# Kernel optimization log

Hardware: AMD Instinct MI355X
Metric: run time of the kernel (lower is better)

## Reference

```python
import jax, jax.numpy as jnp
import numpy as np

EPS = 1e-4
HEADS = 16
DH = 64


def setup_inputs() -> dict:
    key = jax.random.key(0)
    ks = jax.random.split(key, 5)
    b, t, d = 2, 2048, 1024
    return {
        "X": jax.random.normal(ks[0], (b, t, d), dtype=jnp.float32),
        "W_in": jax.random.normal(ks[1], (HEADS * 4 * DH, d), dtype=jnp.float32) * (1.0 / np.sqrt(d)),
        "b_in": jax.random.normal(ks[2], (HEADS * 4 * DH,), dtype=jnp.float32) * 0.01,
        "W_out": jax.random.normal(ks[3], (d, HEADS * DH), dtype=jnp.float32) * (1.0 / np.sqrt(HEADS * DH)),
        "b_out": jax.random.normal(ks[4], (d,), dtype=jnp.float32) * 0.01,
    }


def reference(X, W_in, b_in, W_out, b_out):
    b, t, d = X.shape
    # project_in: [b,t,h*4*dh] -> [b,t,h,4*dh] -> [b,h,t,4*dh]
    P = jnp.einsum('btd,ed->bte', X, W_in) + b_in
    P = P.reshape(b, t, HEADS, 4 * DH).transpose(0, 2, 1, 3)
    Q, K, V, G = jnp.split(P, 4, axis=-1)  # each [b,h,t,dh]
    # Euclidean cdist: sqrt(||q||^2 + ||k||^2 - 2 q.k), clamped at 0
    q2 = jnp.sum(Q * Q, axis=-1)[..., :, None]   # [b,h,t,1]
    k2 = jnp.sum(K * K, axis=-1)[..., None, :]   # [b,h,1,t]
    qk = jnp.einsum('bhqd,bhkd->bhqk', Q, K)
    dist = jnp.sqrt(jnp.maximum(q2 + k2 - 2.0 * qk, 0.0))
    # Shepard weights: (eps + dist)^-2, normalized over keys
    W = (EPS + dist) ** (-2)
    W = W / (EPS + jnp.sum(W, axis=-1, keepdims=True))
    A = jnp.einsum('bhqk,bhkd->bhqd', W, V)
    # gate, merge heads: [b,h,t,dh] -> [b,t,h*dh]
    H = (G * A).transpose(0, 2, 1, 3).reshape(b, t, HEADS * DH)
    Y = jnp.einsum('bte,de->btd', H, W_out) + b_out
    return Y
```

## Files before the change

kernel.cpp:

```cpp
#include <hip/hip_runtime.h>
#include <math.h>

#define EPS 1e-4f


typedef __attribute__((ext_vector_type(8))) short bf16x8;
typedef __attribute__((ext_vector_type(8))) unsigned short u16x8;
typedef __attribute__((ext_vector_type(4))) float f32x4;

#define MFMA(a, b, c) __builtin_amdgcn_mfma_f32_16x16x32_bf16(a, b, c, 0, 0, 0)

__device__ __forceinline__ unsigned short f2b(float f) {
    unsigned int u = __float_as_uint(f);
    u += 0x7fffu + ((u >> 16) & 1u);
    return (unsigned short)(u >> 16);
}
__device__ __forceinline__ float b2f(unsigned short u) {
    return __uint_as_float(((unsigned int)u) << 16);
}
__device__ __forceinline__ unsigned int cvtpk(float a, float b) {
    unsigned int r;
    asm("v_cvt_pk_bf16_f32 %0, %1, %2" : "=v"(r) : "v"(a), "v"(b));
    return r;
}

typedef __attribute__((address_space(1))) const unsigned int as1_u32;
typedef __attribute__((address_space(3))) unsigned int as3_u32;
__device__ __forceinline__ void gl_lds16(const unsigned short* g, unsigned short* l) {
    __builtin_amdgcn_global_load_lds((as1_u32*)g, (as3_u32*)l, 16, 0, 0);
}

__global__ __launch_bounds__(256)
void sga_f2b(const float* __restrict__ src, unsigned short* __restrict__ dst, int n8) {
    int i = blockIdx.x * 256 + threadIdx.x;
    const int stride = gridDim.x * 256;
    for (; i < n8; i += stride) {
        const float4* s = (const float4*)src + i * 2;
        float4 a = s[0], b = s[1];
        uint4 o;
        o.x = (unsigned)f2b(a.x) | ((unsigned)f2b(a.y) << 16);
        o.y = (unsigned)f2b(a.z) | ((unsigned)f2b(a.w) << 16);
        o.z = (unsigned)f2b(b.x) | ((unsigned)f2b(b.y) << 16);
        o.w = (unsigned)f2b(b.z) | ((unsigned)f2b(b.w) << 16);
        *((uint4*)dst + i) = o;
    }
}

__global__ __launch_bounds__(256)
void sga_gemm1(const unsigned short* __restrict__ Xb, const unsigned short* __restrict__ Wb,
               const float* __restrict__ bin,
               unsigned short* __restrict__ Qb, unsigned short* __restrict__ Kb,
               unsigned short* __restrict__ Vt, unsigned short* __restrict__ Gb,
               float* __restrict__ q2s, float* __restrict__ k2s)
{
    __shared__ unsigned short As[128 * 64];
    __shared__ unsigned short Bs[128 * 64];
    const int tid = threadIdx.x;
    const int lane = tid & 63, w = tid >> 6;
    const int lr = lane & 15, lg = lane >> 4;
    const int wm = w & 1, wn = w >> 1;
    const int m0 = blockIdx.y * 128, n0 = blockIdx.x * 128;

    const int sr = tid >> 3, sc8 = tid & 7;
    const int gch = sc8 ^ (sr & 7);
    const unsigned short* aBase = Xb + (m0 + sr) * 1024 + gch * 8;
    const unsigned short* bBase = Wb + (n0 + sr) * 1024 + gch * 8;
    unsigned short* aDst = &As[w * 512];
    unsigned short* bDst = &Bs[w * 512];

    f32x4 acc[4][4] = {};

    for (int kt = 0; kt < 16; ++kt) {
        __syncthreads();
        #pragma unroll
        for (int c = 0; c < 4; ++c)
            gl_lds16(aBase + c * 32768 + kt * 64, aDst + c * 2048);
        #pragma unroll
        for (int c = 0; c < 4; ++c)
            gl_lds16(bBase + c * 32768 + kt * 64, bDst + c * 2048);
        __syncthreads();

        #pragma unroll
        for (int ks = 0; ks < 2; ++ks) {
            bf16x8 af[4], bfr[4];
            #pragma unroll
            for (int i = 0; i < 4; ++i) {
                const int row = wm * 64 + i * 16 + lr;
                af[i] = *(const bf16x8*)&As[row * 64 + (((ks * 4 + lg) ^ (row & 7)) * 8)];
            }
            #pragma unroll
            for (int i = 0; i < 4; ++i) {
                const int row = wn * 64 + i * 16 + lr;
                bfr[i] = *(const bf16x8*)&Bs[row * 64 + (((ks * 4 + lg) ^ (row & 7)) * 8)];
            }
            #pragma unroll
            for (int mi = 0; mi < 4; ++mi)
                #pragma unroll
                for (int ni = 0; ni < 4; ++ni)
                    acc[mi][ni] = MFMA(af[mi], bfr[ni], acc[mi][ni]);
        }
    }

    const int bb = m0 >> 11;
    const bool qkBlock = ((n0 & 128) == 0);
    #pragma unroll
    for (int mf = 0; mf < 4; ++mf) {
        const int tbase = m0 + wm * 64 + mf * 16 + lg * 4;
        const int tloc = tbase & 2047;
        float s2[4] = {0.f, 0.f, 0.f, 0.f};
        #pragma unroll
        for (int nf = 0; nf < 4; ++nf) {
            const int n = n0 + wn * 64 + nf * 16 + lr;
            const int h = n >> 8, cc = n & 255;
            const int part = cc >> 6, j = cc & 63;
            const int bh = bb * 16 + h;
            const float bz = bin[n];
            f32x4 v = acc[mf][nf];
            unsigned short e0 = f2b(v[0] + bz), e1 = f2b(v[1] + bz),
                           e2 = f2b(v[2] + bz), e3 = f2b(v[3] + bz);
            if (qkBlock) {
                float f0 = b2f(e0), f1 = b2f(e1), f2 = b2f(e2), f3 = b2f(e3);
                s2[0] += f0 * f0; s2[1] += f1 * f1;
                s2[2] += f2 * f2; s2[3] += f3 * f3;
            }
            if (part == 2) {
                ushort4 pk = make_ushort4(e0, e1, e2, e3);
                *(ushort4*)&Vt[(bh * 64 + j) * 2048 + tloc] = pk;
            } else {
                unsigned short* dst = (part == 0) ? Qb : ((part == 1) ? Kb : Gb);
                unsigned short vv[4] = {e0, e1, e2, e3};
                #pragma unroll
                for (int r = 0; r < 4; ++r)
                    dst[(bh * 2048 + tloc + r) * 64 + j] = vv[r];
            }
        }
        if (qkBlock) {
            const int bh = bb * 16 + (n0 >> 8);
            float* __restrict__ dstn = wn ? k2s : q2s;
            #pragma unroll
            for (int r = 0; r < 4; ++r) {
                float v = s2[r];
                v += __shfl_xor(v, 1, 64); v += __shfl_xor(v, 2, 64);
                v += __shfl_xor(v, 4, 64); v += __shfl_xor(v, 8, 64);
                if (lr == 0) dstn[bh * 2048 + ((tloc + r) & 2047)] = v;
            }
        }
    }
}

__global__ __launch_bounds__(256, 4)
void sga_attn(const unsigned short* __restrict__ Qb, const unsigned short* __restrict__ Kb,
              const unsigned short* __restrict__ Vt,
              const float* __restrict__ q2s, const float* __restrict__ k2s,
              unsigned short* __restrict__ Op0, unsigned short* __restrict__ Op1,
              unsigned short* __restrict__ Op2, unsigned short* __restrict__ Op3,
              float* __restrict__ Sw0, float* __restrict__ Sw1,
              float* __restrict__ Sw2, float* __restrict__ Sw3)
{
    __shared__ unsigned short Klds[4096];
    __shared__ unsigned short Vlds[4096];
    __shared__ unsigned short Wlds[4 * 2048];

    const int tid = threadIdx.x;
    const int lane = tid & 63, w = tid >> 6;
    const int lr = lane & 15, lg = lane >> 4;

    const int qt = blockIdx.x, bh = blockIdx.y, half = blockIdx.z;
    const int q0 = qt * 128 + w * 32;
    const int kbeg = half * 8, kend = kbeg + 8;

    unsigned short* wl = &Wlds[w * 2048];
    unsigned short* __restrict__ Op =
        (half & 2) ? ((half & 1) ? Op3 : Op2) : ((half & 1) ? Op1 : Op0);
    float* __restrict__ Sw =
        (half & 2) ? ((half & 1) ? Sw3 : Sw2) : ((half & 1) ? Sw1 : Sw0);

    const int sr8 = tid >> 3, sch = tid & 7;
    const int gch = sch ^ (sr8 & 7);
    const unsigned short* Kg = Kb + bh * 2048 * 64;
    const unsigned short* Vg = Vt + bh * 64 * 2048;
    unsigned short* kDst = &Klds[w * 512];
    unsigned short* vDst = &Vlds[w * 512];

    bf16x8 qf[2][2];
    #pragma unroll
    for (int g = 0; g < 2; ++g) {
        const unsigned short* qp = Qb + (bh * 2048 + q0 + g * 16 + lr) * 64 + lg * 8;
        qf[g][0] = *(const bf16x8*)qp;
        qf[g][1] = *(const bf16x8*)(qp + 32);
    }
    float q2v[2];
    q2v[0] = q2s[bh * 2048 + q0 + lr];
    q2v[1] = q2s[bh * 2048 + q0 + 16 + lr];

    f32x4 oacc[2][4] = {};
    float sumw[2] = {0.f, 0.f};

    for (int kt = kbeg; kt < kend; ++kt) {
        const int k0 = kt * 64;

        __syncthreads();
        #pragma unroll
        for (int c = 0; c < 2; ++c) {
            const int row = c * 32 + sr8;
            gl_lds16(Kg + (k0 + row) * 64 + gch * 8, kDst + c * 2048);
            gl_lds16(Vg + row * 2048 + k0 + gch * 8, vDst + c * 2048);
        }
        __syncthreads();

        f32x4 k2v[4];
        #pragma unroll
        for (int nf = 0; nf < 4; ++nf)
            k2v[nf] = *(const f32x4*)&k2s[bh * 2048 + k0 + nf * 16 + lg * 4];

        f32x4 sa[2][4] = {};
        __builtin_amdgcn_s_setprio(1);
        #pragma unroll
        for (int nf = 0; nf < 4; ++nf) {
            const int row = nf * 16 + lr;
            bf16x8 kf0 = *(const bf16x8*)&Klds[row * 64 + ((lg ^ (row & 7)) * 8)];
            bf16x8 kf1 = *(const bf16x8*)&Klds[row * 64 + (((4 + lg) ^ (row & 7)) * 8)];
            #pragma unroll
            for (int g = 0; g < 2; ++g) {
                sa[g][nf] = MFMA(kf0, qf[g][0], sa[g][nf]);
                sa[g][nf] = MFMA(kf1, qf[g][1], sa[g][nf]);
            }
        }
        __builtin_amdgcn_s_setprio(0);

        #pragma unroll
        for (int g = 0; g < 2; ++g) {
            const int row = g * 16 + lr;
            #pragma unroll
            for (int nf = 0; nf < 4; ++nf) {
                float wv[4];
                #pragma unroll
                for (int r = 0; r < 4; ++r) {
                    float d2 = fmaf(-2.0f, sa[g][nf][r], q2v[g] + k2v[nf][r]);
                    d2 = fmaxf(d2, 1e-8f);
                    wv[r] = __builtin_amdgcn_rcpf(d2);
                    sumw[g] += wv[r];
                }
                uint2 pk;
                pk.x = cvtpk(wv[0], wv[1]);
                pk.y = cvtpk(wv[2], wv[3]);
                const int c = 2 * nf + (lg >> 1);
                *(uint2*)&wl[row * 64 + ((c ^ (row & 7)) * 8) + (lg & 1) * 4] = pk;
            }
        }

        bf16x8 pa[2][2];
        #pragma unroll
        for (int g = 0; g < 2; ++g) {
            const int row = g * 16 + lr;
            pa[g][0] = *(const bf16x8*)&wl[row * 64 + ((lg ^ (row & 7)) * 8)];
            pa[g][1] = *(const bf16x8*)&wl[row * 64 + (((4 + lg) ^ (row & 7)) * 8)];
        }
        __builtin_amdgcn_s_setprio(1);
        #pragma unroll
        for (int vf = 0; vf < 4; ++vf) {
            const int row = vf * 16 + lr;
            bf16x8 v0 = *(const bf16x8*)&Vlds[row * 64 + ((lg ^ (row & 7)) * 8)];
            bf16x8 v1 = *(const bf16x8*)&Vlds[row * 64 + (((4 + lg) ^ (row & 7)) * 8)];
            #pragma unroll
            for (int g = 0; g < 2; ++g) {
                oacc[g][vf] = MFMA(pa[g][0], v0, oacc[g][vf]);
                oacc[g][vf] = MFMA(pa[g][1], v1, oacc[g][vf]);
            }
        }
        __builtin_amdgcn_s_setprio(0);
    }

    #pragma unroll
    for (int g = 0; g < 2; ++g) {
        sumw[g] += __shfl_xor(sumw[g], 16, 64);
        sumw[g] += __shfl_xor(sumw[g], 32, 64);
    }

    #pragma unroll
    for (int g = 0; g < 2; ++g) {
        #pragma unroll
        for (int vf = 0; vf < 4; ++vf) {
            #pragma unroll
            for (int r = 0; r < 4; ++r) {
                const int t = q0 + g * 16 + lg * 4 + r;
                const int dh = vf * 16 + lr;
                Op[(bh * 2048 + t) * 64 + dh] = f2b(oacc[g][vf][r]);
            }
        }
    }
    if (lg == 0) {
        Sw[bh * 2048 + q0 + lr]      = sumw[0];
        Sw[bh * 2048 + q0 + 16 + lr] = sumw[1];
    }
}

__global__ __launch_bounds__(256)
void sga_combine(const unsigned short* __restrict__ Op0, const unsigned short* __restrict__ Op1,
                 const unsigned short* __restrict__ Op2, const unsigned short* __restrict__ Op3,
                 const float* __restrict__ Sw0, const float* __restrict__ Sw1,
                 const float* __restrict__ Sw2, const float* __restrict__ Sw3,
                 const unsigned short* __restrict__ Gb, unsigned short* __restrict__ Hb)
{
    const int idx = blockIdx.x * 256 + threadIdx.x;
    const int t16 = idx >> 3;
    const int dq = (idx & 7) << 3;
    u16x8 a = *(const u16x8*)&Op0[t16 * 64 + dq];
    u16x8 b = *(const u16x8*)&Op1[t16 * 64 + dq];
    u16x8 c = *(const u16x8*)&Op2[t16 * 64 + dq];
    u16x8 d = *(const u16x8*)&Op3[t16 * 64 + dq];
    u16x8 g = *(const u16x8*)&Gb[t16 * 64 + dq];
    const float s = Sw0[t16] + Sw1[t16] + Sw2[t16] + Sw3[t16];
    const float inv = __builtin_amdgcn_rcpf(EPS + s);
    const int bh = t16 >> 11, tloc = t16 & 2047;
    const int bb = bh >> 4, h = bh & 15;
    u16x8 o;
    #pragma unroll
    for (int j = 0; j < 8; ++j)
        o[j] = f2b((b2f(a[j]) + b2f(b[j]) + b2f(c[j]) + b2f(d[j])) * inv * b2f(g[j]));
    *(u16x8*)&Hb[(bb * 2048 + tloc) * 1024 + h * 64 + dq] = o;
}

__global__ __launch_bounds__(256)
void sga_gemm2(const unsigned short* __restrict__ Hb, const unsigned short* __restrict__ Wb,
               const float* __restrict__ bout, float* __restrict__ Y)
{
    __shared__ unsigned short As[128 * 64];
    __shared__ unsigned short Bs[128 * 64];
    const int tid = threadIdx.x;
    const int lane = tid & 63, w = tid >> 6;
    const int lr = lane & 15, lg = lane >> 4;
    const int wm = w & 1, wn = w >> 1;
    const int m0 = blockIdx.y * 128, n0 = blockIdx.x * 128;

    const int sr = tid >> 3, sc8 = tid & 7;
    const int gch = sc8 ^ (sr & 7);
    const unsigned short* aBase = Hb + (m0 + sr) * 1024 + gch * 8;
    const unsigned short* bBase = Wb + (n0 + sr) * 1024 + gch * 8;
    unsigned short* aDst = &As[w * 512];
    unsigned short* bDst = &Bs[w * 512];

    f32x4 acc[4][4] = {};

    for (int kt = 0; kt < 16; ++kt) {
        __syncthreads();
        #pragma unroll
        for (int c = 0; c < 4; ++c)
            gl_lds16(aBase + c * 32768 + kt * 64, aDst + c * 2048);
        #pragma unroll
        for (int c = 0; c < 4; ++c)
            gl_lds16(bBase + c * 32768 + kt * 64, bDst + c * 2048);
        __syncthreads();

        #pragma unroll
        for (int ks = 0; ks < 2; ++ks) {
            bf16x8 af[4], bfr[4];
            #pragma unroll
            for (int i = 0; i < 4; ++i) {
                const int row = wm * 64 + i * 16 + lr;
                af[i] = *(const bf16x8*)&As[row * 64 + (((ks * 4 + lg) ^ (row & 7)) * 8)];
            }
            #pragma unroll
            for (int i = 0; i < 4; ++i) {
                const int row = wn * 64 + i * 16 + lr;
                bfr[i] = *(const bf16x8*)&Bs[row * 64 + (((ks * 4 + lg) ^ (row & 7)) * 8)];
            }
            #pragma unroll
            for (int mi = 0; mi < 4; ++mi)
                #pragma unroll
                for (int ni = 0; ni < 4; ++ni)
                    acc[mi][ni] = MFMA(af[mi], bfr[ni], acc[mi][ni]);
        }
    }

    #pragma unroll
    for (int mf = 0; mf < 4; ++mf) {
        const int m = m0 + wm * 64 + mf * 16 + lg * 4;
        #pragma unroll
        for (int nf = 0; nf < 4; ++nf) {
            const int n = n0 + wn * 64 + nf * 16 + lr;
            const float bz = bout[n];
            f32x4 v = acc[mf][nf];
            #pragma unroll
            for (int r = 0; r < 4; ++r)
                Y[(m + r) * 1024 + n] = v[r] + bz;
        }
    }
}

extern "C" void kernel_launch(void* const* d_in, const int* in_sizes, int n_in,
                              void* d_out, int out_size, void* d_ws, size_t ws_size,
                              hipStream_t stream) {
    const float* X    = (const float*)d_in[0];
    const float* Win  = (const float*)d_in[1];
    const float* bin  = (const float*)d_in[2];
    const float* Wout = (const float*)d_in[3];
    const float* bout = (const float*)d_in[4];
    float* Y = (float*)d_out;

    const int PER = 32 * 2048 * 64;
    unsigned short* Qb   = (unsigned short*)d_ws;
    unsigned short* Kb   = Qb + PER;
    unsigned short* Vt   = Kb + PER;
    unsigned short* Gb   = Vt + PER;
    unsigned short* Hb   = Gb + PER;
    unsigned short* Xb   = Hb + PER;
    unsigned short* Winb = Xb + PER;
    unsigned short* Woutb= Winb + PER;
    float* q2s = (float*)(Woutb + 1024 * 1024);
    float* k2s = q2s + 32 * 2048;
    float* Sw0 = k2s + 32 * 2048;
    float* Sw1 = Sw0 + 32 * 2048;
    float* Sw2 = Sw1 + 32 * 2048;
    float* Sw3 = Sw2 + 32 * 2048;
    unsigned short* Op2 = (unsigned short*)(Sw3 + 32 * 2048);
    unsigned short* Op3 = Op2 + PER;
    unsigned short* Op0 = Xb;
    unsigned short* Op1 = Winb;

    sga_f2b<<<1024, 256, 0, stream>>>(X, Xb, 524288);
    sga_f2b<<<1024, 256, 0, stream>>>(Win, Winb, 524288);
    sga_f2b<<<256, 256, 0, stream>>>(Wout, Woutb, 131072);
    sga_gemm1<<<dim3(32, 32), 256, 0, stream>>>(Xb, Winb, bin, Qb, Kb, Vt, Gb, q2s, k2s);
    sga_attn <<<dim3(16, 32, 4), 256, 0, stream>>>(Qb, Kb, Vt, q2s, k2s,
                                                   Op0, Op1, Op2, Op3, Sw0, Sw1, Sw2, Sw3);
    sga_combine<<<2048, 256, 0, stream>>>(Op0, Op1, Op2, Op3, Sw0, Sw1, Sw2, Sw3, Gb, Hb);
    sga_gemm2<<<dim3(8, 32), 256, 0, stream>>>(Hb, Woutb, bout, Y);
}
```

Measured before the change: 166.0 us.

## Double-buffer K/V tiles in LDS to prefetch next tile during compute

The K and V LDS staging buffers are doubled. The next key tile's global-to-LDS loads are issued before computing on the current tile, and the two barriers per iteration become one barrier at the end. This hides global load latency behind the QK and PV MFMA work. The cost is extra LDS per block (about 48KB instead of 32KB), which may lower the number of resident blocks below the launch-bounds target of 4.

```diff
diff --git a/kernel.cpp b/kernel.cpp
--- a/kernel.cpp
+++ b/kernel.cpp
@@ -157,8 +157,8 @@
               float* __restrict__ Sw0, float* __restrict__ Sw1,
               float* __restrict__ Sw2, float* __restrict__ Sw3)
 {
-    __shared__ unsigned short Klds[4096];
-    __shared__ unsigned short Vlds[4096];
+    __shared__ unsigned short Klds[2 * 4096];
+    __shared__ unsigned short Vlds[2 * 4096];
     __shared__ unsigned short Wlds[4 * 2048];
 
     const int tid = threadIdx.x;
@@ -196,17 +196,31 @@
     f32x4 oacc[2][4] = {};
     float sumw[2] = {0.f, 0.f};
 
+    #pragma unroll
+    for (int c = 0; c < 2; ++c) {
+        const int row = c * 32 + sr8;
+        gl_lds16(Kg + (kbeg * 64 + row) * 64 + gch * 8, kDst + c * 2048);
+        gl_lds16(Vg + row * 2048 + kbeg * 64 + gch * 8, vDst + c * 2048);
+    }
+    __syncthreads();
+
+    int buf = 0;
     for (int kt = kbeg; kt < kend; ++kt) {
         const int k0 = kt * 64;
-
-        __syncthreads();
-        #pragma unroll
-        for (int c = 0; c < 2; ++c) {
-            const int row = c * 32 + sr8;
-            gl_lds16(Kg + (k0 + row) * 64 + gch * 8, kDst + c * 2048);
-            gl_lds16(Vg + row * 2048 + k0 + gch * 8, vDst + c * 2048);
-        }
-        __syncthreads();
+        const bool more = (kt + 1 < kend);
+
+        if (more) {
+            const int bo = (buf ^ 1) * 4096;
+            #pragma unroll
+            for (int c = 0; c < 2; ++c) {
+                const int row = c * 32 + sr8;
+                gl_lds16(Kg + ((k0 + 64) + row) * 64 + gch * 8, kDst + bo + c * 2048);
+                gl_lds16(Vg + row * 2048 + (k0 + 64) + gch * 8, vDst + bo + c * 2048);
+            }
+        }
+
+        const unsigned short* kb = &Klds[buf * 4096];
+        const unsigned short* vb = &Vlds[buf * 4096];
 
         f32x4 k2v[4];
         #pragma unroll
@@ -218,8 +232,8 @@
         #pragma unroll
         for (int nf = 0; nf < 4; ++nf) {
             const int row = nf * 16 + lr;
-            bf16x8 kf0 = *(const bf16x8*)&Klds[row * 64 + ((lg ^ (row & 7)) * 8)];
-            bf16x8 kf1 = *(const bf16x8*)&Klds[row * 64 + (((4 + lg) ^ (row & 7)) * 8)];
+            bf16x8 kf0 = *(const bf16x8*)&kb[row * 64 + ((lg ^ (row & 7)) * 8)];
+            bf16x8 kf1 = *(const bf16x8*)&kb[row * 64 + (((4 + lg) ^ (row & 7)) * 8)];
             #pragma unroll
             for (int g = 0; g < 2; ++g) {
                 sa[g][nf] = MFMA(kf0, qf[g][0], sa[g][nf]);
@@ -260,8 +274,8 @@
         #pragma unroll
         for (int vf = 0; vf < 4; ++vf) {
             const int row = vf * 16 + lr;
-            bf16x8 v0 = *(const bf16x8*)&Vlds[row * 64 + ((lg ^ (row & 7)) * 8)];
-            bf16x8 v1 = *(const bf16x8*)&Vlds[row * 64 + (((4 + lg) ^ (row & 7)) * 8)];
+            bf16x8 v0 = *(const bf16x8*)&vb[row * 64 + ((lg ^ (row & 7)) * 8)];
+            bf16x8 v1 = *(const bf16x8*)&vb[row * 64 + (((4 + lg) ^ (row & 7)) * 8)];
             #pragma unroll
             for (int g = 0; g < 2; ++g) {
                 oacc[g][vf] = MFMA(pa[g][0], v0, oacc[g][vf]);
@@ -269,6 +283,11 @@
             }
         }
         __builtin_amdgcn_s_setprio(0);
+
+        if (more) {
+            __syncthreads();
+            buf ^= 1;
+        }
     }
 
     #pragma unroll
```

After: 163.6 us. Within noise of the previous version (-1.5%).
